# Optimization experiments

Measured on AMD Instinct MI355X. Metric: run time of the kernel, lower is better.

Reference implementation:

```python
import jax, jax.numpy as jnp
import numpy as np

B, C, N, RATIO = 16, 1024, 16384, 8
BN_EPS = 1e-5


def setup_inputs() -> dict:
    key = jax.random.key(0)
    k1, k2, k3, k4 = jax.random.split(key, 4)
    return {
        "x": jax.random.normal(k1, (B, C, N), dtype=jnp.float32),
        "w1": jax.random.normal(k2, (C // RATIO, C), dtype=jnp.float32) * (1.0 / np.sqrt(C)),
        "w2": jax.random.normal(k3, (C, C // RATIO), dtype=jnp.float32) * (1.0 / np.sqrt(C // RATIO)),
        "sw": jax.random.normal(k4, (2,), dtype=jnp.float32),
        "gamma": jnp.ones((1,), dtype=jnp.float32),
        "beta": jnp.zeros((1,), dtype=jnp.float32),
        "running_mean": jnp.zeros((1,), dtype=jnp.float32),
        "running_var": jnp.ones((1,), dtype=jnp.float32),
    }


def reference(x, w1, w2, sw, gamma, beta, running_mean, running_var):
    # ---- Channel attention (CBAM) ----
    m = jnp.mean(x, axis=-1)   # (B, C) avg pool over N
    mx = jnp.max(x, axis=-1)   # (B, C) max pool over N

    def mlp(v):  # shared Conv1d(k=1) MLP: C -> C/r -> C
        h = jax.nn.relu(jnp.einsum('rc,bc->br', w1, v))
        return jnp.einsum('cr,br->bc', w2, h)

    gate = jax.nn.sigmoid(mlp(m) + mlp(mx))[:, :, None]  # (B, C, 1)
    x1 = gate * x                                          # (B, C, N)

    # ---- Spatial attention ----
    cm = jnp.mean(x1, axis=1, keepdims=True)  # (B, 1, N) mean over C
    cx = jnp.max(x1, axis=1, keepdims=True)   # (B, 1, N) max over C
    # torch concat order is [max, mean]; conv1 weight sw applies accordingly
    s = sw[0] * cx + sw[1] * cm               # (B, 1, N)
    # BatchNorm1d(1) in eval mode with running stats
    s = (s - running_mean[0]) * jax.lax.rsqrt(running_var[0] + BN_EPS) * gamma[0] + beta[0]
    s = jax.nn.relu(s)
    att = jax.nn.softmax(s, axis=-1)          # softmax over N
    return att * x1                            # (B, C, N)
```

## Files before the change

kernel.cpp:

```cpp
#include <hip/hip_runtime.h>
#include <math.h>

#define BB 16
#define CC 1024
#define NN 16384
#define HID 128
#define SPLIT 4
#define CPART (CC/SPLIT)
#define N4 (NN/4)
#define EXPSHIFT 10.0f
#define CG 8

typedef float f4 __attribute__((ext_vector_type(4)));

__global__ __launch_bounds__(256) void k1_pool(const float* __restrict__ x,
                                               float* __restrict__ meanp,
                                               float* __restrict__ maxp) {
    const int row = blockIdx.x;
    const int tid = threadIdx.x;
    const f4* xr = (const f4*)(x + (size_t)row * NN);
    float s = 0.f, m = -INFINITY;
    #pragma unroll
    for (int i = 0; i < 16; ++i) {
        f4 v = __builtin_nontemporal_load(&xr[tid + i * 256]);
        s += v.x + v.y + v.z + v.w;
        m = fmaxf(m, fmaxf(fmaxf(v.x, v.y), fmaxf(v.z, v.w)));
    }
    __shared__ float ss[4], sm[4];
    for (int off = 32; off > 0; off >>= 1) {
        s += __shfl_down(s, off, 64);
        m = fmaxf(m, __shfl_down(m, off, 64));
    }
    const int wave = tid >> 6, lane = tid & 63;
    if (lane == 0) { ss[wave] = s; sm[wave] = m; }
    __syncthreads();
    if (tid == 0) {
        float fs = ss[0] + ss[1] + ss[2] + ss[3];
        float fm = fmaxf(fmaxf(sm[0], sm[1]), fmaxf(sm[2], sm[3]));
        meanp[row] = fs * (1.0f / NN);
        maxp[row]  = fm;
    }
}

__global__ __launch_bounds__(1024) void k2_gate(const float* __restrict__ meanp,
                                                const float* __restrict__ maxp,
                                                const float* __restrict__ w1,
                                                const float* __restrict__ w2,
                                                float* __restrict__ gate) {
    const int b = blockIdx.x;
    const int tid = threadIdx.x;
    __shared__ float sv[2][CC];
    __shared__ float hh[2][HID];
    __shared__ float h[HID];
    if (tid < CC) {
        sv[0][tid] = meanp[b * CC + tid];
        sv[1][tid] = maxp[b * CC + tid];
    }
    __syncthreads();
    {
        const int slot = tid >> 2;
        const int part = tid & 3;
        const int src  = slot >> 7;
        const int r    = slot & 127;
        const float* w1r = w1 + (size_t)r * CC;
        const float* svp = sv[src];
        float acc = 0.f;
        const int c0 = part * 256;
        #pragma unroll 8
        for (int c = c0; c < c0 + 256; ++c) acc = fmaf(w1r[c], svp[c], acc);
        acc += __shfl_xor(acc, 1, 64);
        acc += __shfl_xor(acc, 2, 64);
        if (part == 0) hh[src][r] = fmaxf(acc, 0.f);
    }
    __syncthreads();
    if (tid < HID) h[tid] = hh[0][tid] + hh[1][tid];
    __syncthreads();
    {
        const float* w2r = w2 + (size_t)tid * HID;
        float a = 0.f;
        #pragma unroll
        for (int r = 0; r < HID; ++r) a = fmaf(w2r[r], h[r], a);
        gate[b * CC + tid] = 1.0f / (1.0f + expf(-a));
    }
}

__global__ __launch_bounds__(256) void k3_spatial(const float* __restrict__ x,
                                                  const float* __restrict__ gate,
                                                  float* __restrict__ psum,
                                                  float* __restrict__ pmax) {
    const int chunk = blockIdx.x;
    const int split = blockIdx.y;
    const int b     = blockIdx.z;
    const int tid = threadIdx.x;
    __shared__ float g[CPART];
    g[tid] = gate[b * CC + split * CPART + tid];
    __syncthreads();
    const int n4 = chunk * 256 + tid;
    const f4* xb = (const f4*)(x + ((size_t)b * CC + (size_t)split * CPART) * NN);
    f4 s = {0.f, 0.f, 0.f, 0.f};
    f4 m = {-INFINITY, -INFINITY, -INFINITY, -INFINITY};
    #pragma unroll 16
    for (int c = 0; c < CPART; ++c) {
        f4 v = __builtin_nontemporal_load(&xb[(size_t)c * N4 + n4]);
        float gc = g[c];
        s.x = fmaf(gc, v.x, s.x);
        s.y = fmaf(gc, v.y, s.y);
        s.z = fmaf(gc, v.z, s.z);
        s.w = fmaf(gc, v.w, s.w);
        m.x = fmaxf(m.x, gc * v.x);
        m.y = fmaxf(m.y, gc * v.y);
        m.z = fmaxf(m.z, gc * v.z);
        m.w = fmaxf(m.w, gc * v.w);
    }
    const size_t o = (size_t)(b * SPLIT + split) * N4 + n4;
    ((f4*)psum)[o] = s;
    ((f4*)pmax)[o] = m;
}

__global__ __launch_bounds__(256) void k4_exp(const float* __restrict__ psum,
                                              const float* __restrict__ pmax,
                                              const float* __restrict__ sw,
                                              const float* __restrict__ gamma,
                                              const float* __restrict__ beta,
                                              const float* __restrict__ rmean,
                                              const float* __restrict__ rvar,
                                              float* __restrict__ attexp,
                                              float* __restrict__ blksum) {
    const int chunk = blockIdx.x;
    const int b     = blockIdx.y;
    const int tid = threadIdx.x;
    const float sw0 = sw[0], sw1 = sw[1];
    const float scale = gamma[0] * rsqrtf(rvar[0] + 1e-5f);
    const float shift = beta[0] - rmean[0] * scale;
    const int i = chunk * 256 + tid;
    const f4* ps = (const f4*)psum;
    const f4* pm = (const f4*)pmax;
    f4 ssum = {0.f, 0.f, 0.f, 0.f};
    f4 smax = {-INFINITY, -INFINITY, -INFINITY, -INFINITY};
    #pragma unroll
    for (int sp = 0; sp < SPLIT; ++sp) {
        f4 a = ps[(size_t)(b * SPLIT + sp) * N4 + i];
        f4 c = pm[(size_t)(b * SPLIT + sp) * N4 + i];
        ssum.x += a.x; ssum.y += a.y; ssum.z += a.z; ssum.w += a.w;
        smax.x = fmaxf(smax.x, c.x); smax.y = fmaxf(smax.y, c.y);
        smax.z = fmaxf(smax.z, c.z); smax.w = fmaxf(smax.w, c.w);
    }
    auto sval = [&](float su, float mx) -> float {
        float v = sw0 * mx + sw1 * (su * (1.0f / CC));
        v = fmaf(v, scale, shift);
        v = fmaxf(v, 0.f);
        return expf(v - EXPSHIFT);
    };
    f4 e;
    e.x = sval(ssum.x, smax.x);
    e.y = sval(ssum.y, smax.y);
    e.z = sval(ssum.z, smax.z);
    e.w = sval(ssum.w, smax.w);
    ((f4*)attexp)[(size_t)b * N4 + i] = e;
    float lsum = e.x + e.y + e.z + e.w;
    for (int off = 32; off > 0; off >>= 1) lsum += __shfl_down(lsum, off, 64);
    __shared__ float red[4];
    if ((tid & 63) == 0) red[tid >> 6] = lsum;
    __syncthreads();
    if (tid == 0) blksum[b * 16 + chunk] = red[0] + red[1] + red[2] + red[3];
}

__global__ __launch_bounds__(256) void k5_gscale(const float* __restrict__ gate,
                                                 const float* __restrict__ blksum,
                                                 float* __restrict__ gscale) {
    const int row = blockIdx.x * 256 + threadIdx.x;
    const int b = row >> 10;
    float tot = 0.f;
    #pragma unroll
    for (int j = 0; j < 16; ++j) tot += blksum[b * 16 + j];
    gscale[row] = gate[row] / tot;
}

__global__ __launch_bounds__(256) void k6_final(const float* __restrict__ x,
                                                const float* __restrict__ gscale,
                                                const float* __restrict__ attexp,
                                                float* __restrict__ out) {
    const int chunk = blockIdx.x;
    const int cgrp  = blockIdx.y;
    const int b     = blockIdx.z;
    const int tid = threadIdx.x;
    const int n4 = chunk * 256 + tid;
    const int row0 = b * CC + cgrp * CG;
    const f4 a = ((const f4*)attexp)[(size_t)b * N4 + n4];
    float gs[CG];
    #pragma unroll
    for (int r = 0; r < CG; ++r) gs[r] = gscale[row0 + r];
    const f4* xp = (const f4*)x;
    f4* op = (f4*)out;
    f4 v[CG];
    #pragma unroll
    for (int r = 0; r < CG; ++r)
        v[r] = __builtin_nontemporal_load(&xp[(size_t)(row0 + r) * N4 + n4]);
    #pragma unroll
    for (int r = 0; r < CG; ++r) {
        f4 o;
        o.x = v[r].x * a.x * gs[r];
        o.y = v[r].y * a.y * gs[r];
        o.z = v[r].z * a.z * gs[r];
        o.w = v[r].w * a.w * gs[r];
        __builtin_nontemporal_store(o, &op[(size_t)(row0 + r) * N4 + n4]);
    }
}

extern "C" void kernel_launch(void* const* d_in, const int* in_sizes, int n_in,
                              void* d_out, int out_size, void* d_ws, size_t ws_size,
                              hipStream_t stream) {
    const float* x     = (const float*)d_in[0];
    const float* w1    = (const float*)d_in[1];
    const float* w2    = (const float*)d_in[2];
    const float* sw    = (const float*)d_in[3];
    const float* gamma = (const float*)d_in[4];
    const float* beta  = (const float*)d_in[5];
    const float* rmean = (const float*)d_in[6];
    const float* rvar  = (const float*)d_in[7];
    float* out = (float*)d_out;
    float* ws  = (float*)d_ws;

    float* meanp  = ws;
    float* maxp   = meanp + 16384;
    float* gate   = maxp + 16384;
    float* gscale = gate + 16384;
    float* psum   = gscale + 16384;
    float* pmax   = psum + (size_t)BB * SPLIT * NN;
    float* attexp = pmax + (size_t)BB * SPLIT * NN;
    float* blksum = attexp + (size_t)BB * NN;

    k1_pool<<<BB * CC, 256, 0, stream>>>(x, meanp, maxp);
    k2_gate<<<BB, 1024, 0, stream>>>(meanp, maxp, w1, w2, gate);
    dim3 g3(NN / 1024, SPLIT, BB);
    k3_spatial<<<g3, 256, 0, stream>>>(x, gate, psum, pmax);
    dim3 g4(16, BB);
    k4_exp<<<g4, 256, 0, stream>>>(psum, pmax, sw, gamma, beta, rmean, rvar, attexp, blksum);
    k5_gscale<<<BB * CC / 256, 256, 0, stream>>>(gate, blksum, gscale);
    dim3 g6(16, CC / CG, BB);
    k6_final<<<g6, 256, 0, stream>>>(x, gscale, attexp, out);
}
```

Measured before the change: 758.8 us.

## Process batches in L2-sized groups so x is re-read from cache

Result: slower. 1.163 ms (+53.3%).

```diff
diff --git a/kernel.cpp b/kernel.cpp
--- a/kernel.cpp
+++ b/kernel.cpp
@@ -5,8 +5,11 @@
 #define CC 1024
 #define NN 16384
 #define HID 128
-#define SPLIT 4
-#define CPART (CC/SPLIT)
+#define GROUP 2
+#define NGROUPS (BB/GROUP)
+#define SPLIT 16
+#define CROWS (CC/SPLIT)
+#define NSPL 16
 #define N4 (NN/4)
 #define EXPSHIFT 10.0f
 #define CG 8
@@ -15,14 +18,15 @@
 
 __global__ __launch_bounds__(256) void k1_pool(const float* __restrict__ x,
                                                float* __restrict__ meanp,
-                                               float* __restrict__ maxp) {
-    const int row = blockIdx.x;
+                                               float* __restrict__ maxp,
+                                               int b0) {
+    const int row = b0 * CC + blockIdx.x;
     const int tid = threadIdx.x;
     const f4* xr = (const f4*)(x + (size_t)row * NN);
     float s = 0.f, m = -INFINITY;
     #pragma unroll
     for (int i = 0; i < 16; ++i) {
-        f4 v = __builtin_nontemporal_load(&xr[tid + i * 256]);
+        f4 v = xr[tid + i * 256];
         s += v.x + v.y + v.z + v.w;
         m = fmaxf(m, fmaxf(fmaxf(v.x, v.y), fmaxf(v.z, v.w)));
     }
@@ -46,8 +50,9 @@
                                                 const float* __restrict__ maxp,
                                                 const float* __restrict__ w1,
                                                 const float* __restrict__ w2,
-                                                float* __restrict__ gate) {
-    const int b = blockIdx.x;
+                                                float* __restrict__ gate,
+                                                int b0) {
+    const int b = b0 + blockIdx.x;
     const int tid = threadIdx.x;
     __shared__ float sv[2][CC];
     __shared__ float hh[2][HID];
@@ -87,21 +92,22 @@
 __global__ __launch_bounds__(256) void k3_spatial(const float* __restrict__ x,
                                                   const float* __restrict__ gate,
                                                   float* __restrict__ psum,
-                                                  float* __restrict__ pmax) {
-    const int chunk = blockIdx.x;
+                                                  float* __restrict__ pmax,
+                                                  int b0) {
+    const int npart = blockIdx.x;
     const int split = blockIdx.y;
-    const int b     = blockIdx.z;
-    const int tid = threadIdx.x;
-    __shared__ float g[CPART];
-    g[tid] = gate[b * CC + split * CPART + tid];
-    __syncthreads();
-    const int n4 = chunk * 256 + tid;
-    const f4* xb = (const f4*)(x + ((size_t)b * CC + (size_t)split * CPART) * NN);
+    const int b     = b0 + blockIdx.z;
+    const int tid = threadIdx.x;
+    __shared__ float g[CROWS];
+    if (tid < CROWS) g[tid] = gate[b * CC + split * CROWS + tid];
+    __syncthreads();
+    const int n4 = npart * 256 + tid;
+    const f4* xb = (const f4*)(x + ((size_t)b * CC + (size_t)split * CROWS) * NN);
     f4 s = {0.f, 0.f, 0.f, 0.f};
     f4 m = {-INFINITY, -INFINITY, -INFINITY, -INFINITY};
-    #pragma unroll 16
-    for (int c = 0; c < CPART; ++c) {
-        f4 v = __builtin_nontemporal_load(&xb[(size_t)c * N4 + n4]);
+    #pragma unroll 8
+    for (int c = 0; c < CROWS; ++c) {
+        f4 v = xb[(size_t)c * N4 + n4];
         float gc = g[c];
         s.x = fmaf(gc, v.x, s.x);
         s.y = fmaf(gc, v.y, s.y);
@@ -125,9 +131,10 @@
                                               const float* __restrict__ rmean,
                                               const float* __restrict__ rvar,
                                               float* __restrict__ attexp,
-                                              float* __restrict__ blksum) {
+                                              float* __restrict__ blksum,
+                                              int b0) {
     const int chunk = blockIdx.x;
-    const int b     = blockIdx.y;
+    const int b     = b0 + blockIdx.y;
     const int tid = threadIdx.x;
     const float sw0 = sw[0], sw1 = sw[1];
     const float scale = gamma[0] * rsqrtf(rvar[0] + 1e-5f);
@@ -165,37 +172,32 @@
     if (tid == 0) blksum[b * 16 + chunk] = red[0] + red[1] + red[2] + red[3];
 }
 
-__global__ __launch_bounds__(256) void k5_gscale(const float* __restrict__ gate,
-                                                 const float* __restrict__ blksum,
-                                                 float* __restrict__ gscale) {
-    const int row = blockIdx.x * 256 + threadIdx.x;
-    const int b = row >> 10;
-    float tot = 0.f;
-    #pragma unroll
-    for (int j = 0; j < 16; ++j) tot += blksum[b * 16 + j];
-    gscale[row] = gate[row] / tot;
-}
-
 __global__ __launch_bounds__(256) void k6_final(const float* __restrict__ x,
-                                                const float* __restrict__ gscale,
+                                                const float* __restrict__ gate,
+                                                const float* __restrict__ blksum,
                                                 const float* __restrict__ attexp,
-                                                float* __restrict__ out) {
+                                                float* __restrict__ out,
+                                                int b0) {
     const int chunk = blockIdx.x;
     const int cgrp  = blockIdx.y;
-    const int b     = blockIdx.z;
+    const int b     = b0 + blockIdx.z;
     const int tid = threadIdx.x;
     const int n4 = chunk * 256 + tid;
     const int row0 = b * CC + cgrp * CG;
+    float tot = 0.f;
+    #pragma unroll
+    for (int j = 0; j < 16; ++j) tot += blksum[b * 16 + j];
+    const float inv = 1.0f / tot;
     const f4 a = ((const f4*)attexp)[(size_t)b * N4 + n4];
     float gs[CG];
     #pragma unroll
-    for (int r = 0; r < CG; ++r) gs[r] = gscale[row0 + r];
+    for (int r = 0; r < CG; ++r) gs[r] = gate[row0 + r] * inv;
     const f4* xp = (const f4*)x;
     f4* op = (f4*)out;
     f4 v[CG];
     #pragma unroll
     for (int r = 0; r < CG; ++r)
-        v[r] = __builtin_nontemporal_load(&xp[(size_t)(row0 + r) * N4 + n4]);
+        v[r] = xp[(size_t)(row0 + r) * N4 + n4];
     #pragma unroll
     for (int r = 0; r < CG; ++r) {
         f4 o;
@@ -224,19 +226,20 @@
     float* meanp  = ws;
     float* maxp   = meanp + 16384;
     float* gate   = maxp + 16384;
-    float* gscale = gate + 16384;
-    float* psum   = gscale + 16384;
+    float* psum   = gate + 16384;
     float* pmax   = psum + (size_t)BB * SPLIT * NN;
     float* attexp = pmax + (size_t)BB * SPLIT * NN;
     float* blksum = attexp + (size_t)BB * NN;
 
-    k1_pool<<<BB * CC, 256, 0, stream>>>(x, meanp, maxp);
-    k2_gate<<<BB, 1024, 0, stream>>>(meanp, maxp, w1, w2, gate);
-    dim3 g3(NN / 1024, SPLIT, BB);
-    k3_spatial<<<g3, 256, 0, stream>>>(x, gate, psum, pmax);
-    dim3 g4(16, BB);
-    k4_exp<<<g4, 256, 0, stream>>>(psum, pmax, sw, gamma, beta, rmean, rvar, attexp, blksum);
-    k5_gscale<<<BB * CC / 256, 256, 0, stream>>>(gate, blksum, gscale);
-    dim3 g6(16, CC / CG, BB);
-    k6_final<<<g6, 256, 0, stream>>>(x, gscale, attexp, out);
-}
+    for (int g = 0; g < NGROUPS; ++g) {
+        const int b0 = g * GROUP;
+        k1_pool<<<GROUP * CC, 256, 0, stream>>>(x, meanp, maxp, b0);
+        k2_gate<<<GROUP, 1024, 0, stream>>>(meanp, maxp, w1, w2, gate, b0);
+        dim3 g3(NSPL, SPLIT, GROUP);
+        k3_spatial<<<g3, 256, 0, stream>>>(x, gate, psum, pmax, b0);
+        dim3 g4(16, GROUP);
+        k4_exp<<<g4, 256, 0, stream>>>(psum, pmax, sw, gamma, beta, rmean, rvar, attexp, blksum, b0);
+        dim3 g6(16, CC / CG, GROUP);
+        k6_final<<<g6, 256, 0, stream>>>(x, gate, blksum, attexp, out, b0);
+    }
+}
```
